# Performance work log

Measured on AMD Instinct MI355X. Metric: run time of the kernel, lower is better.

The kernel has to match this reference:

```python
import jax, jax.numpy as jnp
import numpy as np

N_NODES = 50000
N_EDGES = 800000
N_GRAPHS = 64
IN_CH = 128
HID_CH = 128
FC_CH = 128


def setup_inputs() -> dict:
    key = jax.random.key(0)
    ks = jax.random.split(key, 12)

    def lin_w(k, fan_in, fan_out):
        return jax.random.normal(k, (fan_in, fan_out), jnp.float32) * (1.0 / np.sqrt(fan_in))

    return {
        "x": jax.random.normal(ks[0], (N_NODES, IN_CH), jnp.float32),
        "edge_index": jax.random.randint(ks[1], (2, N_EDGES), 0, N_NODES, dtype=jnp.int64),
        "batch_vec": jnp.sort(jax.random.randint(ks[2], (N_NODES,), 0, N_GRAPHS, dtype=jnp.int64)),
        "W1": lin_w(ks[3], IN_CH, HID_CH),
        "b1": jnp.zeros((HID_CH,), jnp.float32),
        "W2": lin_w(ks[4], HID_CH, HID_CH),
        "b2": jnp.zeros((HID_CH,), jnp.float32),
        "W3": lin_w(ks[5], HID_CH, FC_CH),
        "b3": jnp.zeros((FC_CH,), jnp.float32),
        "fcW1": lin_w(ks[6], FC_CH, IN_CH),
        "fcb1": jnp.zeros((IN_CH,), jnp.float32),
        "fcW2": lin_w(ks[7], IN_CH, 2),
        "fcb2": jnp.zeros((2,), jnp.float32),
    }


def reference(x, edge_index, batch_vec, W1, b1, W2, b2, W3, b3, fcW1, fcb1, fcW2, fcb2):
    n = x.shape[0]
    row, col = edge_index[0], edge_index[1]  # src -> dst

    # GCN symmetric normalization with self-loops: deg[j] = in-degree(j) + 1
    deg = jnp.zeros((n,), x.dtype).at[col].add(1.0) + 1.0
    inv_sqrt = jax.lax.rsqrt(deg)
    edge_norm = inv_sqrt[row] * inv_sqrt[col]  # [E]
    self_norm = (inv_sqrt * inv_sqrt)[:, None]  # [N,1], self-loop weight 1/deg

    def gcn(h, W, b):
        h = h @ W  # [N, out]
        agg = jnp.zeros_like(h).at[col].add(h[row] * edge_norm[:, None])
        return agg + h * self_norm + b

    h = jax.nn.relu(gcn(x, W1, b1))
    h = jax.nn.relu(gcn(h, W2, b2))
    h = jax.nn.relu(gcn(h, W3, b3))
    h = jax.nn.relu(h @ fcW1 + fcb1)
    h = h @ fcW2 + fcb2  # [N, 2]

    # global mean pool per graph
    sums = jax.ops.segment_sum(h, batch_vec, num_segments=N_GRAPHS)
    cnts = jax.ops.segment_sum(jnp.ones((n,), h.dtype), batch_vec, num_segments=N_GRAPHS)
    pooled = sums / jnp.maximum(cnts, 1.0)[:, None]  # [G, 2]
    return jax.nn.softmax(pooled, axis=1)
```

## Files before the change

### kernel.cpp

```cpp
#include <hip/hip_runtime.h>


#define CH 128
#define BSH 7
#define SEG 4096
#define EPW 4096
#define SA 40
#define SC 132
#define SC8 144

typedef unsigned short ushortT;
typedef unsigned int uintT;
typedef unsigned char ucharT;
typedef __attribute__((ext_vector_type(8))) short short8;
typedef __attribute__((ext_vector_type(4))) float floatx4;
typedef __attribute__((ext_vector_type(2))) float floatx2;

__device__ __forceinline__ float bf2f(uintT u) {
    return __uint_as_float(u << 16);
}
__device__ __forceinline__ ushortT f2bf(float f) {
    uintT x = __float_as_uint(f);
    return (ushortT)((x + 0x7fffu + ((x >> 16) & 1u)) >> 16);
}
__device__ __forceinline__ void dec4(uintT u, float* o) {
    floatx2 lo = __builtin_amdgcn_cvt_pk_f32_fp8((int)u, false);
    floatx2 hi = __builtin_amdgcn_cvt_pk_f32_fp8((int)u, true);
    o[0] = lo.x; o[1] = lo.y; o[2] = hi.x; o[3] = hi.y;
}

__global__ void k_zero(int* __restrict__ bfill, int NB, float* __restrict__ acc, int nacc) {
    int t = threadIdx.x;
    for (int i = t; i < NB; i += 256) bfill[i] = 0;
    for (int i = t; i < nacc; i += 256) acc[i] = 0.f;
}

__global__ __launch_bounds__(256) void k_bin(const int* __restrict__ row,
                                             const int* __restrict__ col,
                                             int* __restrict__ bfill,
                                             uintT* __restrict__ seg,
                                             int E, int NB) {
    __shared__ uintT staged[EPW];
    __shared__ int target[EPW];
    __shared__ int sval[512];
    __shared__ int horig[512];
    __shared__ int pcnt[512];
    __shared__ int gbase[512];
    const int t = threadIdx.x;
    const int e0 = blockIdx.x * EPW;
    const int cnt = min(EPW, E - e0);

    sval[t] = 0; sval[t + 256] = 0;
    __syncthreads();

    int er[16], ec[16];
#pragma unroll
    for (int i = 0; i < 16; ++i) {
        int le = i * 256 + t;
        if (le < cnt) {
            er[i] = row[e0 + le];
            ec[i] = col[e0 + le];
            atomicAdd(&sval[ec[i] >> BSH], 1);
        }
    }
    __syncthreads();
    horig[t] = sval[t]; horig[t + 256] = sval[t + 256];
    __syncthreads();
    for (int off = 1; off < 512; off <<= 1) {
        int a = (t >= off) ? sval[t - off] : 0;
        int b2 = sval[t + 256 - off];
        __syncthreads();
        sval[t] += a;
        sval[t + 256] += b2;
        __syncthreads();
    }
    for (int b = t; b < 512; b += 256) {
        int h = horig[b];
        pcnt[b] = sval[b] - h;
        gbase[b] = (h > 0 && b < NB) ? atomicAdd(&bfill[b], h) : 0;
    }
    __syncthreads();
#pragma unroll
    for (int i = 0; i < 16; ++i) {
        int le = i * 256 + t;
        if (le < cnt) {
            int b = ec[i] >> BSH;
            int j = atomicAdd(&pcnt[b], 1);
            staged[j] = (uintT)er[i] | ((uintT)ec[i] << 16);
            int lo = sval[b] - horig[b];
            target[j] = b * SEG + gbase[b] + (j - lo);
        }
    }
    __syncthreads();
    for (int s = t; s < cnt; s += 256) seg[target[s]] = staged[s];
}

__global__ __launch_bounds__(512) void k_binvs_bscan(const int* __restrict__ bfill,
                                                     const uintT* __restrict__ seg,
                                                     float* __restrict__ invs,
                                                     int* __restrict__ bbase,
                                                     int* __restrict__ indptr,
                                                     int NB, int N, int E) {
    const int b = blockIdx.x;
    const int t = threadIdx.x;
    if (b < NB) {
        __shared__ int h[128];
        if (t < 128) h[t] = 0;
        __syncthreads();
        int cnt = bfill[b];
        const uintT* sp = seg + (size_t)b * SEG;
        for (int s = t; s < cnt; s += 512) atomicAdd(&h[(sp[s] >> 16) & 127], 1);
        __syncthreads();
        int d = b * 128 + t;
        if (t < 128 && d < N) invs[d] = rsqrtf((float)h[t] + 1.0f);
    } else {
        __shared__ int s[512];
        int v = (t < NB) ? bfill[t] : 0;
        s[t] = v;
        __syncthreads();
        for (int off = 1; off < 512; off <<= 1) {
            int a = (t >= off) ? s[t - off] : 0;
            __syncthreads();
            s[t] += a;
            __syncthreads();
        }
        if (t < NB) bbase[t] = s[t] - v;
        if (t == 0) indptr[N] = E;
    }
}

__global__ __launch_bounds__(256) void k_scatterprep(const int* __restrict__ bfill,
                                                     const int* __restrict__ bbase,
                                                     const uintT* __restrict__ seg,
                                                     const float* __restrict__ invs,
                                                     int* __restrict__ indptr,
                                                     uintT* __restrict__ epack,
                                                     const float* __restrict__ X,
                                                     ucharT* __restrict__ Xb,
                                                     const float* __restrict__ w0,
                                                     const float* __restrict__ w1,
                                                     const float* __restrict__ w2,
                                                     const float* __restrict__ w3,
                                                     ushortT* __restrict__ Whi,
                                                     int N, int NB, int total4) {
    const int t = threadIdx.x;
    if ((int)blockIdx.x < NB) {
        __shared__ uintT staged[SEG];
        __shared__ int h[128];
        __shared__ int sc[128];
        __shared__ int pc[128];
        const int b = blockIdx.x;
        const int cnt = bfill[b];
        const int base = bbase[b];
        const uintT* sp = seg + (size_t)b * SEG;

        if (t < 128) h[t] = 0;
        __syncthreads();
        for (int s = t; s < cnt; s += 256) atomicAdd(&h[(sp[s] >> 16) & 127], 1);
        __syncthreads();
        if (t < 128) sc[t] = h[t];
        __syncthreads();
        for (int off = 1; off < 128; off <<= 1) {
            int a = (t >= off && t < 128) ? sc[t - off] : 0;
            __syncthreads();
            if (t < 128) sc[t] += a;
            __syncthreads();
        }
        if (t < 128) {
            int excl = sc[t] - h[t];
            pc[t] = excl;
            int d = b * 128 + t;
            if (d < N) indptr[d] = base + excl;
        }
        __syncthreads();
        for (int s = t; s < cnt; s += 256) {
            uintT rc = sp[s];
            int src = (int)(rc & 0xffffu), dst = (int)(rc >> 16);
            int j = atomicAdd(&pc[dst & 127], 1);
            float nrm = invs[src] * invs[dst];
            staged[j] = (uintT)src | ((uintT)f2bf(nrm) << 16);
        }
        __syncthreads();
        for (int s = t; s < cnt; s += 256) epack[base + s] = staged[s];
    } else if ((int)blockIdx.x < NB + 256) {
        int idx = (blockIdx.x - NB) * 256 + t;
        int m = idx >> 14;
        int r = idx & 16383;
        int n = r >> 7;
        int k = r & 127;
        const float* W = (m == 0) ? w0 : (m == 1) ? w1 : (m == 2) ? w2 : w3;
        Whi[m * 16384 + n * CH + k] = f2bf(W[k * CH + n]);
    } else {
        int i = (blockIdx.x - NB - 256) * 256 + t;
        if (i < total4) {
            float4 v = reinterpret_cast<const float4*>(X)[i];
            int r0 = __builtin_amdgcn_cvt_pk_fp8_f32(v.x, v.y, 0, false);
            int r1 = __builtin_amdgcn_cvt_pk_fp8_f32(v.z, v.w, r0, true);
            reinterpret_cast<int*>(Xb)[i] = r1;
        }
    }
}

__global__ __launch_bounds__(256) void k_agg(const ucharT* __restrict__ H8,
                                             const uintT* __restrict__ epack,
                                             const int* __restrict__ indptr,
                                             const float* __restrict__ invs,
                                             ucharT* __restrict__ Z8, int N) {
    const int wave = threadIdx.x >> 6, lane = threadIdx.x & 63;
    const int sub = lane >> 4;
    const int l = lane & 15;
    const int node = blockIdx.x * 16 + wave * 4 + sub;
    if (node >= N) return;

    const uint2* H2 = reinterpret_cast<const uint2*>(H8);

    float acc[8];
    {
        float sn = invs[node];
        float sn2 = sn * sn;
        uint2 h = H2[(size_t)node * 16 + l];
        float d[8];
        dec4(h.x, d); dec4(h.y, d + 4);
#pragma unroll
        for (int j = 0; j < 8; ++j) acc[j] = sn2 * d[j];
    }

    int p = indptr[node];
    int p1 = indptr[node + 1];
    for (; p + 8 <= p1; p += 8) {
        uintT e[8];
#pragma unroll
        for (int i = 0; i < 8; ++i) e[i] = epack[p + i];
        uint2 g[8];
#pragma unroll
        for (int i = 0; i < 8; ++i) g[i] = H2[(size_t)(int)(e[i] & 0xffffu) * 16 + l];
#pragma unroll
        for (int i = 0; i < 8; ++i) {
            float wv = bf2f(e[i] >> 16);
            float d[8];
            dec4(g[i].x, d); dec4(g[i].y, d + 4);
#pragma unroll
            for (int j = 0; j < 8; ++j) acc[j] += wv * d[j];
        }
    }
    if (p + 4 <= p1) {
        uintT e[4];
#pragma unroll
        for (int i = 0; i < 4; ++i) e[i] = epack[p + i];
        uint2 g[4];
#pragma unroll
        for (int i = 0; i < 4; ++i) g[i] = H2[(size_t)(int)(e[i] & 0xffffu) * 16 + l];
#pragma unroll
        for (int i = 0; i < 4; ++i) {
            float wv = bf2f(e[i] >> 16);
            float d[8];
            dec4(g[i].x, d); dec4(g[i].y, d + 4);
#pragma unroll
            for (int j = 0; j < 8; ++j) acc[j] += wv * d[j];
        }
        p += 4;
    }
    for (; p < p1; ++p) {
        uintT e = epack[p];
        uint2 g = H2[(size_t)(int)(e & 0xffffu) * 16 + l];
        float wv = bf2f(e >> 16);
        float d[8];
        dec4(g.x, d); dec4(g.y, d + 4);
#pragma unroll
        for (int j = 0; j < 8; ++j) acc[j] += wv * d[j];
    }

    uint2 o;
    {
        int r0 = __builtin_amdgcn_cvt_pk_fp8_f32(acc[0], acc[1], 0, false);
        r0 = __builtin_amdgcn_cvt_pk_fp8_f32(acc[2], acc[3], r0, true);
        int r1 = __builtin_amdgcn_cvt_pk_fp8_f32(acc[4], acc[5], 0, false);
        r1 = __builtin_amdgcn_cvt_pk_fp8_f32(acc[6], acc[7], r1, true);
        o.x = (uintT)r0; o.y = (uintT)r1;
    }
    reinterpret_cast<uint2*>(Z8)[(size_t)node * 16 + l] = o;
}

__global__ __launch_bounds__(256) void k_gemm(const void* __restrict__ InV,
                                              const ushortT* __restrict__ Whi,
                                              const float* __restrict__ Bias,
                                              void* __restrict__ OutV, int N,
                                              int inFp8, int outFp8) {
    __shared__ ushortT smem[128 * SC];
    ushortT* As = smem;
    ushortT* Ws = smem + 128 * SA;
    ushortT* Cs = smem;

    const int tid = threadIdx.x;
    const int wave = tid >> 6, lane = tid & 63;
    const int quad = lane >> 4, l15 = lane & 15;
    const int mBase = (wave >> 1) * 64, nBase = (wave & 1) * 64;
    const int row0 = blockIdx.x * 128;
    const int r = tid >> 1, half = tid & 1;

    floatx4 acc[4][4];
    const floatx4 zero4 = {0.f, 0.f, 0.f, 0.f};
#pragma unroll
    for (int i = 0; i < 4; i++)
#pragma unroll
        for (int j = 0; j < 4; j++) acc[i][j] = zero4;

    for (int ks = 0; ks < 4; ++ks) {
        {
            int grow = row0 + r;
            if (inFp8) {
                uint4 a8 = {0, 0, 0, 0};
                if (grow < N)
                    a8 = *reinterpret_cast<const uint4*>(
                        (const ucharT*)InV + (size_t)grow * CH + ks * 32 + half * 16);
                uintT wds[4] = {a8.x, a8.y, a8.z, a8.w};
                uintT ob[8];
#pragma unroll
                for (int q = 0; q < 4; ++q) {
                    float d[4];
                    dec4(wds[q], d);
                    ob[2 * q] = (uintT)f2bf(d[0]) | ((uintT)f2bf(d[1]) << 16);
                    ob[2 * q + 1] = (uintT)f2bf(d[2]) | ((uintT)f2bf(d[3]) << 16);
                }
                uint4* dd = reinterpret_cast<uint4*>(&As[r * SA + half * 16]);
                dd[0] = uint4{ob[0], ob[1], ob[2], ob[3]};
                dd[1] = uint4{ob[4], ob[5], ob[6], ob[7]};
            } else {
                uint4 av0 = {0, 0, 0, 0}, av1 = {0, 0, 0, 0};
                if (grow < N) {
                    const uint4* s = reinterpret_cast<const uint4*>(
                        (const ushortT*)InV + (size_t)grow * CH + ks * 32 + half * 16);
                    av0 = s[0]; av1 = s[1];
                }
                uint4* d = reinterpret_cast<uint4*>(&As[r * SA + half * 16]);
                d[0] = av0; d[1] = av1;
            }
            const uint4* sh = reinterpret_cast<const uint4*>(Whi + r * CH + ks * 32 + half * 16);
            uint4* dh = reinterpret_cast<uint4*>(&Ws[r * SA + half * 16]);
            dh[0] = sh[0]; dh[1] = sh[1];
        }
        __syncthreads();

        short8 af[4], wf[4];
#pragma unroll
        for (int mt = 0; mt < 4; ++mt)
            af[mt] = *reinterpret_cast<const short8*>(&As[(mBase + mt * 16 + l15) * SA + quad * 8]);
#pragma unroll
        for (int nt = 0; nt < 4; ++nt)
            wf[nt] = *reinterpret_cast<const short8*>(&Ws[(nBase + nt * 16 + l15) * SA + quad * 8]);
#pragma unroll
        for (int mt = 0; mt < 4; ++mt)
#pragma unroll
            for (int nt = 0; nt < 4; ++nt)
                acc[mt][nt] = __builtin_amdgcn_mfma_f32_16x16x32_bf16(af[mt], wf[nt], acc[mt][nt], 0, 0, 0);
        __syncthreads();
    }

    float bb[4];
#pragma unroll
    for (int nt = 0; nt < 4; ++nt) bb[nt] = Bias[nBase + nt * 16 + l15];

    if (outFp8) {
        ucharT* Cs8 = reinterpret_cast<ucharT*>(Cs);
#pragma unroll
        for (int mt = 0; mt < 4; ++mt)
#pragma unroll
            for (int nt = 0; nt < 4; ++nt)
#pragma unroll
                for (int r4 = 0; r4 < 4; ++r4) {
                    int lrow = mBase + mt * 16 + quad * 4 + r4;
                    float v = fmaxf(acc[mt][nt][r4] + bb[nt], 0.f);
                    int f8 = __builtin_amdgcn_cvt_pk_fp8_f32(v, 0.f, 0, false);
                    Cs8[lrow * SC8 + nBase + nt * 16 + l15] = (ucharT)(f8 & 0xff);
                }
        __syncthreads();
        int grow = row0 + r;
        if (grow < N) {
            const uint4* s4 = reinterpret_cast<const uint4*>(&Cs8[r * SC8 + half * 64]);
            uint4* dst = reinterpret_cast<uint4*>((ucharT*)OutV + (size_t)grow * CH + half * 64);
#pragma unroll
            for (int q = 0; q < 4; ++q) dst[q] = s4[q];
        }
    } else {
        ushortT* Out = (ushortT*)OutV;
#pragma unroll
        for (int mt = 0; mt < 4; ++mt)
#pragma unroll
            for (int nt = 0; nt < 4; ++nt)
#pragma unroll
                for (int r4 = 0; r4 < 4; ++r4) {
                    int lrow = mBase + mt * 16 + quad * 4 + r4;
                    float v = fmaxf(acc[mt][nt][r4] + bb[nt], 0.f);
                    Cs[lrow * SC + nBase + nt * 16 + l15] = f2bf(v);
                }
        __syncthreads();
        int grow = row0 + r;
        if (grow < N) {
            const uint2* s = reinterpret_cast<const uint2*>(&Cs[r * SC + half * 64]);
            uint4* dst = reinterpret_cast<uint4*>(Out + (size_t)grow * CH + half * 64);
#pragma unroll
            for (int q = 0; q < 8; ++q) {
                uint2 a = s[2 * q], b = s[2 * q + 1];
                uint4 o = {a.x, a.y, b.x, b.y};
                dst[q] = o;
            }
        }
    }
}

__global__ __launch_bounds__(256) void k_fc2pool(const ushortT* __restrict__ H,
                                                 const float* __restrict__ W2,
                                                 const float* __restrict__ B2,
                                                 const int* __restrict__ batch,
                                                 float* __restrict__ sums,
                                                 float* __restrict__ cnts, int N) {
    __shared__ float ls[192];
    const int t = threadIdx.x;
    if (t < 192) ls[t] = 0.f;
    __syncthreads();
    const int wave = t >> 6, lane = t & 63;
    const int sub = lane & 7;
    const int ng = lane >> 3;

    float w0[16], w1[16];
#pragma unroll
    for (int i = 0; i < 16; ++i) {
        float2 wv = *reinterpret_cast<const float2*>(W2 + (sub * 16 + i) * 2);
        w0[i] = wv.x;
        w1[i] = wv.y;
    }
    const float b0 = B2[0], b1 = B2[1];

    const int nodeBase = blockIdx.x * 256 + wave * 64;
#pragma unroll
    for (int it = 0; it < 8; ++it) {
        int node = nodeBase + it * 8 + ng;
        float d0 = 0.f, d1 = 0.f;
        if (node < N) {
            const uint4* hp = reinterpret_cast<const uint4*>(H + (size_t)node * CH + sub * 16);
            uint4 a = hp[0], b = hp[1];
            uintT uu[8] = {a.x, a.y, a.z, a.w, b.x, b.y, b.z, b.w};
#pragma unroll
            for (int q = 0; q < 8; ++q) {
                float h0 = bf2f(uu[q] & 0xffffu);
                float h1 = bf2f(uu[q] >> 16);
                d0 += h0 * w0[2 * q] + h1 * w0[2 * q + 1];
                d1 += h0 * w1[2 * q] + h1 * w1[2 * q + 1];
            }
        }
#pragma unroll
        for (int m = 4; m >= 1; m >>= 1) {
            d0 += __shfl_xor(d0, m, 64);
            d1 += __shfl_xor(d1, m, 64);
        }
        if (sub == 0 && node < N) {
            int g = batch[node];
            atomicAdd(&ls[g], d0 + b0);
            atomicAdd(&ls[64 + g], d1 + b1);
            atomicAdd(&ls[128 + g], 1.0f);
        }
    }
    __syncthreads();
    if (t < 64) {
        float c = ls[128 + t];
        if (c != 0.f) {
            atomicAdd(&sums[2 * t], ls[t]);
            atomicAdd(&sums[2 * t + 1], ls[64 + t]);
            atomicAdd(&cnts[t], c);
        }
    }
}

__global__ void k_softmax(const float* __restrict__ sums, const float* __restrict__ cnts,
                          float* __restrict__ out, int G) {
    int g = blockIdx.x * blockDim.x + threadIdx.x;
    if (g < G) {
        float c = fmaxf(cnts[g], 1.0f);
        float p0 = sums[2 * g] / c;
        float p1 = sums[2 * g + 1] / c;
        float m = fmaxf(p0, p1);
        float e0 = expf(p0 - m), e1 = expf(p1 - m);
        float inv = 1.f / (e0 + e1);
        out[2 * g] = e0 * inv;
        out[2 * g + 1] = e1 * inv;
    }
}

extern "C" void kernel_launch(void* const* d_in, const int* in_sizes, int n_in,
                              void* d_out, int out_size, void* d_ws, size_t ws_size,
                              hipStream_t stream) {
    const float* X   = (const float*)d_in[0];
    const int* EI    = (const int*)d_in[1];
    const int* BATCH = (const int*)d_in[2];
    const float* W1  = (const float*)d_in[3];
    const float* B1  = (const float*)d_in[4];
    const float* W2  = (const float*)d_in[5];
    const float* B2  = (const float*)d_in[6];
    const float* W3  = (const float*)d_in[7];
    const float* B3  = (const float*)d_in[8];
    const float* FW1 = (const float*)d_in[9];
    const float* FB1 = (const float*)d_in[10];
    const float* FW2 = (const float*)d_in[11];
    const float* FB2 = (const float*)d_in[12];

    const int N = in_sizes[0] / CH;
    const int E = in_sizes[1] / 2;
    const int G = out_size / 2;
    const int* rowp = EI;
    const int* colp = EI + E;
    const int NB = (N + 127) >> BSH;

    char* w = (char*)d_ws;
    auto alloc = [&](size_t bytes) -> char* {
        char* p = w;
        w += (bytes + 255) & ~(size_t)255;
        return p;
    };
    ushortT* Zb    = (ushortT*)alloc((size_t)N * CH * 2);
    ushortT* Hb16  = (ushortT*)alloc((size_t)N * CH * 2);
    ucharT*  Z8    = (ucharT*)alloc((size_t)N * CH);
    ucharT*  Hb8   = (ucharT*)alloc((size_t)N * CH);
    ucharT*  Xb8   = (ucharT*)alloc((size_t)N * CH);
    ushortT* WhiA  = (ushortT*)alloc((size_t)4 * 16384 * 2);
    float* invs    = (float*)alloc((size_t)N * 4);
    int*   indptr  = (int*)alloc((size_t)(N + 1) * 4);
    uintT* epack   = (uintT*)alloc((size_t)E * 4);
    uintT* seg     = (uintT*)alloc((size_t)NB * SEG * 4);
    int*   bfill   = (int*)alloc((size_t)NB * 4);
    int*   bbase   = (int*)alloc((size_t)NB * 4);
    float* sums    = (float*)alloc((size_t)G * 3 * 4);
    float* cnts    = sums + 2 * G;

    const int nbAgg  = (N + 15) / 16;
    const int nbGemm = (N + 127) / 128;
    const int nbBin  = (E + EPW - 1) / EPW;
    const int nbPool = (N + 255) / 256;
    const int total4 = N * CH / 4;
    const int nbSP   = NB + 256 + (total4 + 255) / 256;

    k_zero<<<1, 256, 0, stream>>>(bfill, NB, sums, 3 * G);
    k_bin<<<nbBin, 256, 0, stream>>>(rowp, colp, bfill, seg, E, NB);
    k_binvs_bscan<<<NB + 1, 512, 0, stream>>>(bfill, seg, invs, bbase, indptr, NB, N, E);
    k_scatterprep<<<nbSP, 256, 0, stream>>>(bfill, bbase, seg, invs, indptr, epack,
                                            X, Xb8, W1, W2, W3, FW1, WhiA, N, NB, total4);

    k_agg<<<nbAgg, 256, 0, stream>>>(Xb8, epack, indptr, invs, Z8, N);
    k_gemm<<<nbGemm, 256, 0, stream>>>(Z8, WhiA, B1, Hb8, N, 1, 1);
    k_agg<<<nbAgg, 256, 0, stream>>>(Hb8, epack, indptr, invs, Z8, N);
    k_gemm<<<nbGemm, 256, 0, stream>>>(Z8, WhiA + 16384, B2, Hb8, N, 1, 1);
    k_agg<<<nbAgg, 256, 0, stream>>>(Hb8, epack, indptr, invs, Z8, N);
    k_gemm<<<nbGemm, 256, 0, stream>>>(Z8, WhiA + 2 * 16384, B3, Hb16, N, 1, 0);
    k_gemm<<<nbGemm, 256, 0, stream>>>(Hb16, WhiA + 3 * 16384, FB1, Zb, N, 0, 0);
    k_fc2pool<<<nbPool, 256, 0, stream>>>(Zb, FW2, FB2, BATCH, sums, cnts, N);
    k_softmax<<<1, 64, 0, stream>>>(sums, cnts, (float*)d_out, G);
}
```

Baseline: 228.0 us.

## Fuse layer-3 GEMM, FC1 GEMM, FC2 and pooling into one tail kernel

Replaces the last two GEMM launches and the separate FC2+pool kernel with a single kernel. The layer-3 output tile stays in shared memory as bf16 and feeds the FC1 GEMM directly. FC2 and the per-graph pooling are then done from registers via shuffle reductions. This removes two bf16 N×128 intermediate round trips through global memory and two launches, at the cost of more shared memory per block, which may lower occupancy.

```diff
diff --git a/kernel.cpp b/kernel.cpp
--- a/kernel.cpp
+++ b/kernel.cpp
@@ -6,6 +6,7 @@
 #define SEG 4096
 #define EPW 4096
 #define SA 40
+#define SAF 136
 #define SC 132
 #define SC8 144
 
@@ -281,11 +282,10 @@
     reinterpret_cast<uint2*>(Z8)[(size_t)node * 16 + l] = o;
 }
 
-__global__ __launch_bounds__(256) void k_gemm(const void* __restrict__ InV,
+__global__ __launch_bounds__(256) void k_gemm(const ucharT* __restrict__ In8,
                                               const ushortT* __restrict__ Whi,
                                               const float* __restrict__ Bias,
-                                              void* __restrict__ OutV, int N,
-                                              int inFp8, int outFp8) {
+                                              ucharT* __restrict__ Out8, int N) {
     __shared__ ushortT smem[128 * SC];
     ushortT* As = smem;
     ushortT* Ws = smem + 128 * SA;
@@ -308,33 +308,22 @@
     for (int ks = 0; ks < 4; ++ks) {
         {
             int grow = row0 + r;
-            if (inFp8) {
-                uint4 a8 = {0, 0, 0, 0};
-                if (grow < N)
-                    a8 = *reinterpret_cast<const uint4*>(
-                        (const ucharT*)InV + (size_t)grow * CH + ks * 32 + half * 16);
-                uintT wds[4] = {a8.x, a8.y, a8.z, a8.w};
-                uintT ob[8];
-#pragma unroll
-                for (int q = 0; q < 4; ++q) {
-                    float d[4];
-                    dec4(wds[q], d);
-                    ob[2 * q] = (uintT)f2bf(d[0]) | ((uintT)f2bf(d[1]) << 16);
-                    ob[2 * q + 1] = (uintT)f2bf(d[2]) | ((uintT)f2bf(d[3]) << 16);
-                }
-                uint4* dd = reinterpret_cast<uint4*>(&As[r * SA + half * 16]);
-                dd[0] = uint4{ob[0], ob[1], ob[2], ob[3]};
-                dd[1] = uint4{ob[4], ob[5], ob[6], ob[7]};
-            } else {
-                uint4 av0 = {0, 0, 0, 0}, av1 = {0, 0, 0, 0};
-                if (grow < N) {
-                    const uint4* s = reinterpret_cast<const uint4*>(
-                        (const ushortT*)InV + (size_t)grow * CH + ks * 32 + half * 16);
-                    av0 = s[0]; av1 = s[1];
-                }
-                uint4* d = reinterpret_cast<uint4*>(&As[r * SA + half * 16]);
-                d[0] = av0; d[1] = av1;
+            uint4 a8 = {0, 0, 0, 0};
+            if (grow < N)
+                a8 = *reinterpret_cast<const uint4*>(
+                    In8 + (size_t)grow * CH + ks * 32 + half * 16);
+            uintT wds[4] = {a8.x, a8.y, a8.z, a8.w};
+            uintT ob[8];
+#pragma unroll
+            for (int q = 0; q < 4; ++q) {
+                float d[4];
+                dec4(wds[q], d);
+                ob[2 * q] = (uintT)f2bf(d[0]) | ((uintT)f2bf(d[1]) << 16);
+                ob[2 * q + 1] = (uintT)f2bf(d[2]) | ((uintT)f2bf(d[3]) << 16);
             }
+            uint4* dd = reinterpret_cast<uint4*>(&As[r * SA + half * 16]);
+            dd[0] = uint4{ob[0], ob[1], ob[2], ob[3]};
+            dd[1] = uint4{ob[4], ob[5], ob[6], ob[7]};
             const uint4* sh = reinterpret_cast<const uint4*>(Whi + r * CH + ks * 32 + half * 16);
             uint4* dh = reinterpret_cast<uint4*>(&Ws[r * SA + half * 16]);
             dh[0] = sh[0]; dh[1] = sh[1];
@@ -360,8 +349,106 @@
 #pragma unroll
     for (int nt = 0; nt < 4; ++nt) bb[nt] = Bias[nBase + nt * 16 + l15];
 
-    if (outFp8) {
-        ucharT* Cs8 = reinterpret_cast<ucharT*>(Cs);
+    ucharT* Cs8 = reinterpret_cast<ucharT*>(Cs);
+#pragma unroll
+    for (int mt = 0; mt < 4; ++mt)
+#pragma unroll
+        for (int nt = 0; nt < 4; ++nt)
+#pragma unroll
+            for (int r4 = 0; r4 < 4; ++r4) {
+                int lrow = mBase + mt * 16 + quad * 4 + r4;
+                float v = fmaxf(acc[mt][nt][r4] + bb[nt], 0.f);
+                int f8 = __builtin_amdgcn_cvt_pk_fp8_f32(v, 0.f, 0, false);
+                Cs8[lrow * SC8 + nBase + nt * 16 + l15] = (ucharT)(f8 & 0xff);
+            }
+    __syncthreads();
+    {
+        int grow = row0 + r;
+        if (grow < N) {
+            const uint4* s4 = reinterpret_cast<const uint4*>(&Cs8[r * SC8 + half * 64]);
+            uint4* dst = reinterpret_cast<uint4*>(Out8 + (size_t)grow * CH + half * 64);
+#pragma unroll
+            for (int q = 0; q < 4; ++q) dst[q] = s4[q];
+        }
+    }
+}
+
+__global__ __launch_bounds__(256) void k_tail(const ucharT* __restrict__ Z8,
+                                              const ushortT* __restrict__ W3hi,
+                                              const float* __restrict__ B3,
+                                              const ushortT* __restrict__ F1hi,
+                                              const float* __restrict__ FB1,
+                                              const float* __restrict__ FW2,
+                                              const float* __restrict__ FB2,
+                                              const int* __restrict__ batch,
+                                              float* __restrict__ sums,
+                                              float* __restrict__ cnts, int N) {
+    __shared__ ushortT Hf[128 * SAF];
+    __shared__ ushortT Ws[128 * SA];
+    __shared__ float rp0[256];
+    __shared__ float rp1[256];
+    __shared__ float ls[192];
+
+    const int tid = threadIdx.x;
+    const int wave = tid >> 6, lane = tid & 63;
+    const int quad = lane >> 4, l15 = lane & 15;
+    const int mBase = (wave >> 1) * 64, nBase = (wave & 1) * 64;
+    const int row0 = blockIdx.x * 128;
+    const int r = tid >> 1, half = tid & 1;
+
+    {
+        int grow = row0 + r;
+        uint4 a8 = {0, 0, 0, 0}, b8 = {0, 0, 0, 0}, c8 = {0, 0, 0, 0}, d8v = {0, 0, 0, 0};
+        if (grow < N) {
+            const uint4* s = reinterpret_cast<const uint4*>(Z8 + (size_t)grow * CH + half * 64);
+            a8 = s[0]; b8 = s[1]; c8 = s[2]; d8v = s[3];
+        }
+        uintT wds[16] = {a8.x, a8.y, a8.z, a8.w, b8.x, b8.y, b8.z, b8.w,
+                         c8.x, c8.y, c8.z, c8.w, d8v.x, d8v.y, d8v.z, d8v.w};
+#pragma unroll
+        for (int q = 0; q < 16; ++q) {
+            float d[4];
+            dec4(wds[q], d);
+            uint2 o;
+            o.x = (uintT)f2bf(d[0]) | ((uintT)f2bf(d[1]) << 16);
+            o.y = (uintT)f2bf(d[2]) | ((uintT)f2bf(d[3]) << 16);
+            *reinterpret_cast<uint2*>(&Hf[r * SAF + half * 64 + q * 4]) = o;
+        }
+    }
+
+    floatx4 acc[4][4];
+    const floatx4 zero4 = {0.f, 0.f, 0.f, 0.f};
+#pragma unroll
+    for (int i = 0; i < 4; i++)
+#pragma unroll
+        for (int j = 0; j < 4; j++) acc[i][j] = zero4;
+
+    for (int ks = 0; ks < 4; ++ks) {
+        {
+            const uint4* sh = reinterpret_cast<const uint4*>(W3hi + r * CH + ks * 32 + half * 16);
+            uint4* dh = reinterpret_cast<uint4*>(&Ws[r * SA + half * 16]);
+            dh[0] = sh[0]; dh[1] = sh[1];
+        }
+        __syncthreads();
+        short8 af[4], wf[4];
+#pragma unroll
+        for (int mt = 0; mt < 4; ++mt)
+            af[mt] = *reinterpret_cast<const short8*>(&Hf[(mBase + mt * 16 + l15) * SAF + ks * 32 + quad * 8]);
+#pragma unroll
+        for (int nt = 0; nt < 4; ++nt)
+            wf[nt] = *reinterpret_cast<const short8*>(&Ws[(nBase + nt * 16 + l15) * SA + quad * 8]);
+#pragma unroll
+        for (int mt = 0; mt < 4; ++mt)
+#pragma unroll
+            for (int nt = 0; nt < 4; ++nt)
+                acc[mt][nt] = __builtin_amdgcn_mfma_f32_16x16x32_bf16(af[mt], wf[nt], acc[mt][nt], 0, 0, 0);
+        __syncthreads();
+    }
+
+    {
+        float bb[4];
+#pragma unroll
+        for (int nt = 0; nt < 4; ++nt) bb[nt] = B3[nBase + nt * 16 + l15];
 #pragma unroll
         for (int mt = 0; mt < 4; ++mt)
 #pragma unroll
@@ -370,103 +457,92 @@
                 for (int r4 = 0; r4 < 4; ++r4) {
                     int lrow = mBase + mt * 16 + quad * 4 + r4;
                     float v = fmaxf(acc[mt][nt][r4] + bb[nt], 0.f);
-                    int f8 = __builtin_amdgcn_cvt_pk_fp8_f32(v, 0.f, 0, false);
-                    Cs8[lrow * SC8 + nBase + nt * 16 + l15] = (ucharT)(f8 & 0xff);
+                    Hf[lrow * SAF + nBase + nt * 16 + l15] = f2bf(v);
                 }
-        __syncthreads();
-        int grow = row0 + r;
-        if (grow < N) {
-            const uint4* s4 = reinterpret_cast<const uint4*>(&Cs8[r * SC8 + half * 64]);
-            uint4* dst = reinterpret_cast<uint4*>((ucharT*)OutV + (size_t)grow * CH + half * 64);
-#pragma unroll
-            for (int q = 0; q < 4; ++q) dst[q] = s4[q];
-        }
-    } else {
-        ushortT* Out = (ushortT*)OutV;
+    }
+    __syncthreads();
+
+#pragma unroll
+    for (int i = 0; i < 4; i++)
+#pragma unroll
+        for (int j = 0; j < 4; j++) acc[i][j] = zero4;
+    for (int ks = 0; ks < 4; ++ks) {
+        {
+            const uint4* sh = reinterpret_cast<const uint4*>(F1hi + r * CH + ks * 32 + half * 16);
+            uint4* dh = reinterpret_cast<uint4*>(&Ws[r * SA + half * 16]);
+            dh[0] = sh[0]; dh[1] = sh[1];
+        }
+        __syncthreads();
+        short8 af[4], wf[4];
+#pragma unroll
+        for (int mt = 0; mt < 4; ++mt)
+            af[mt] = *reinterpret_cast<const short8*>(&Hf[(mBase + mt * 16 + l15) * SAF + ks * 32 + quad * 8]);
+#pragma unroll
+        for (int nt = 0; nt < 4; ++nt)
+            wf[nt] = *reinterpret_cast<const short8*>(&Ws[(nBase + nt * 16 + l15) * SA + quad * 8]);
 #pragma unroll
         for (int mt = 0; mt < 4; ++mt)
 #pragma unroll
             for (int nt = 0; nt < 4; ++nt)
-#pragma unroll
-                for (int r4 = 0; r4 < 4; ++r4) {
+                acc[mt][nt] = __builtin_amdgcn_mfma_f32_16x16x32_bf16(af[mt], wf[nt], acc[mt][nt], 0, 0, 0);
+        __syncthreads();
+    }
+
+    {
+        float bb[4];
+#pragma unroll
+        for (int nt = 0; nt < 4; ++nt) bb[nt] = FB1[nBase + nt * 16 + l15];
+        float w20[4], w21[4];
+#pragma unroll
+        for (int nt = 0; nt < 4; ++nt) {
+            float2 wv = *reinterpret_cast<const float2*>(FW2 + 2 * (nBase + nt * 16 + l15));
+            w20[nt] = wv.x;
+            w21[nt] = wv.y;
+        }
+#pragma unroll
+        for (int mt = 0; mt < 4; ++mt)
+#pragma unroll
+            for (int r4 = 0; r4 < 4; ++r4) {
+                float d0 = 0.f, d1 = 0.f;
+#pragma unroll
+                for (int nt = 0; nt < 4; ++nt) {
+                    float v = fmaxf(acc[mt][nt][r4] + bb[nt], 0.f);
+                    d0 += v * w20[nt];
+                    d1 += v * w21[nt];
+                }
+#pragma unroll
+                for (int m = 8; m >= 1; m >>= 1) {
+                    d0 += __shfl_xor(d0, m, 64);
+                    d1 += __shfl_xor(d1, m, 64);
+                }
+                if (l15 == 0) {
                     int lrow = mBase + mt * 16 + quad * 4 + r4;
-                    float v = fmaxf(acc[mt][nt][r4] + bb[nt], 0.f);
-                    Cs[lrow * SC + nBase + nt * 16 + l15] = f2bf(v);
+                    rp0[lrow * 2 + (wave & 1)] = d0;
+                    rp1[lrow * 2 + (wave & 1)] = d1;
                 }
-        __syncthreads();
-        int grow = row0 + r;
-        if (grow < N) {
-            const uint2* s = reinterpret_cast<const uint2*>(&Cs[r * SC + half * 64]);
-            uint4* dst = reinterpret_cast<uint4*>(Out + (size_t)grow * CH + half * 64);
-#pragma unroll
-            for (int q = 0; q < 8; ++q) {
-                uint2 a = s[2 * q], b = s[2 * q + 1];
-                uint4 o = {a.x, a.y, b.x, b.y};
-                dst[q] = o;
             }
-        }
-    }
-}
-
-__global__ __launch_bounds__(256) void k_fc2pool(const ushortT* __restrict__ H,
-                                                 const float* __restrict__ W2,
-                                                 const float* __restrict__ B2,
-                                                 const int* __restrict__ batch,
-                                                 float* __restrict__ sums,
-                                                 float* __restrict__ cnts, int N) {
-    __shared__ float ls[192];
-    const int t = threadIdx.x;
-    if (t < 192) ls[t] = 0.f;
-    __syncthreads();
-    const int wave = t >> 6, lane = t & 63;
-    const int sub = lane & 7;
-    const int ng = lane >> 3;
-
-    float w0[16], w1[16];
-#pragma unroll
-    for (int i = 0; i < 16; ++i) {
-        float2 wv = *reinterpret_cast<const float2*>(W2 + (sub * 16 + i) * 2);
-        w0[i] = wv.x;
-        w1[i] = wv.y;
-    }
-    const float b0 = B2[0], b1 = B2[1];
-
-    const int nodeBase = blockIdx.x * 256 + wave * 64;
-#pragma unroll
-    for (int it = 0; it < 8; ++it) {
-        int node = nodeBase + it * 8 + ng;
-        float d0 = 0.f, d1 = 0.f;
+    }
+    if (tid < 192) ls[tid] = 0.f;
+    __syncthreads();
+
+    if (tid < 128) {
+        int node = row0 + tid;
         if (node < N) {
-            const uint4* hp = reinterpret_cast<const uint4*>(H + (size_t)node * CH + sub * 16);
-            uint4 a = hp[0], b = hp[1];
-            uintT uu[8] = {a.x, a.y, a.z, a.w, b.x, b.y, b.z, b.w};
-#pragma unroll
-            for (int q = 0; q < 8; ++q) {
-                float h0 = bf2f(uu[q] & 0xffffu);
-                float h1 = bf2f(uu[q] >> 16);
-                d0 += h0 * w0[2 * q] + h1 * w0[2 * q + 1];
-                d1 += h0 * w1[2 * q] + h1 * w1[2 * q + 1];
-            }
-        }
-#pragma unroll
-        for (int m = 4; m >= 1; m >>= 1) {
-            d0 += __shfl_xor(d0, m, 64);
-            d1 += __shfl_xor(d1, m, 64);
-        }
-        if (sub == 0 && node < N) {
+            float d0 = rp0[tid * 2] + rp0[tid * 2 + 1] + FB2[0];
+            float d1 = rp1[tid * 2] + rp1[tid * 2 + 1] + FB2[1];
             int g = batch[node];
-            atomicAdd(&ls[g], d0 + b0);
-            atomicAdd(&ls[64 + g], d1 + b1);
+            atomicAdd(&ls[g], d0);
+            atomicAdd(&ls[64 + g], d1);
             atomicAdd(&ls[128 + g], 1.0f);
         }
     }
     __syncthreads();
-    if (t < 64) {
-        float c = ls[128 + t];
+    if (tid < 64) {
+        float c = ls[128 + tid];
         if (c != 0.f) {
-            atomicAdd(&sums[2 * t], ls[t]);
-            atomicAdd(&sums[2 * t + 1], ls[64 + t]);
-            atomicAdd(&cnts[t], c);
+            atomicAdd(&sums[2 * tid], ls[tid]);
+            atomicAdd(&sums[2 * tid + 1], ls[64 + tid]);
+            atomicAdd(&cnts[tid], c);
         }
     }
 }
@@ -516,8 +592,6 @@
         w += (bytes + 255) & ~(size_t)255;
         return p;
     };
-    ushortT* Zb    = (ushortT*)alloc((size_t)N * CH * 2);
-    ushortT* Hb16  = (ushortT*)alloc((size_t)N * CH * 2);
     ucharT*  Z8    = (ucharT*)alloc((size_t)N * CH);
     ucharT*  Hb8   = (ucharT*)alloc((size_t)N * CH);
     ucharT*  Xb8   = (ucharT*)alloc((size_t)N * CH);
@@ -534,7 +608,6 @@
     const int nbAgg  = (N + 15) / 16;
     const int nbGemm = (N + 127) / 128;
     const int nbBin  = (E + EPW - 1) / EPW;
-    const int nbPool = (N + 255) / 256;
     const int total4 = N * CH / 4;
     const int nbSP   = NB + 256 + (total4 + 255) / 256;
 
@@ -545,12 +618,12 @@
                                             X, Xb8, W1, W2, W3, FW1, WhiA, N, NB, total4);
 
     k_agg<<<nbAgg, 256, 0, stream>>>(Xb8, epack, indptr, invs, Z8, N);
-    k_gemm<<<nbGemm, 256, 0, stream>>>(Z8, WhiA, B1, Hb8, N, 1, 1);
+    k_gemm<<<nbGemm, 256, 0, stream>>>(Z8, WhiA, B1, Hb8, N);
     k_agg<<<nbAgg, 256, 0, stream>>>(Hb8, epack, indptr, invs, Z8, N);
-    k_gemm<<<nbGemm, 256, 0, stream>>>(Z8, WhiA + 16384, B2, Hb8, N, 1, 1);
+    k_gemm<<<nbGemm, 256, 0, stream>>>(Z8, WhiA + 16384, B2, Hb8, N);
     k_agg<<<nbAgg, 256, 0, stream>>>(Hb8, epack, indptr, invs, Z8, N);
-    k_gemm<<<nbGemm, 256, 0, stream>>>(Z8, WhiA + 2 * 16384, B3, Hb16, N, 1, 0);
-    k_gemm<<<nbGemm, 256, 0, stream>>>(Hb16, WhiA + 3 * 16384, FB1, Zb, N, 0, 0);
-    k_fc2pool<<<nbPool, 256, 0, stream>>>(Zb, FW2, FB2, BATCH, sums, cnts, N);
+    k_tail<<<nbGemm, 256, 0, stream>>>(Z8, WhiA + 2 * 16384, B3,
+                                       WhiA + 3 * 16384, FB1, FW2, FB2,
+                                       BATCH, sums, cnts, N);
     k_softmax<<<1, 64, 0, stream>>>(sums, cnts, (float*)d_out, G);
 }
```

Result: faster. 211.7 us (-7.2%).
